# Kernel optimization log

Hardware: AMD Instinct MI355X
Metric: run time of the kernel (lower is better)

## Reference

```python
import jax, jax.numpy as jnp
import numpy as np

N_FEATURES = 200
KERNEL = 50
N_WIN = N_FEATURES - KERNEL + 1  # 151 sub-vectors
HID_F = [100, 50]
HID_G = [50, 25]   # 0.5 * hidden_dims
REP = 128
BATCH = 2048
TAU = 0.01
BN_EPS = 1e-5


def _window_indices():
    start = np.arange(N_FEATURES)[:-KERNEL + 1]
    all_idx = start[:, None] + np.arange(KERNEL)                      # [N_WIN, KERNEL]
    comp = np.array([np.setdiff1d(np.arange(N_FEATURES), row) for row in all_idx])  # [N_WIN, N_FEATURES-KERNEL]
    return jnp.asarray(all_idx), jnp.asarray(comp)

ALL_IDX, COMP_IDX = _window_indices()


def setup_inputs() -> dict:
    key = jax.random.key(0)
    ks = jax.random.split(key, 8)
    def w(k, o, i):
        return jax.random.normal(k, (o, i), jnp.float32) / np.float32(np.sqrt(i))
    gd = [KERNEL] + HID_G + [REP]
    fd = [N_FEATURES - KERNEL] + HID_F + [REP]
    inp = {"x": jax.random.normal(ks[0], (BATCH, N_FEATURES), jnp.float32)}
    inp["gW0"] = w(ks[1], gd[1], gd[0])
    inp["gW1"] = w(ks[2], gd[2], gd[1])
    inp["gW2"] = w(ks[3], gd[3], gd[2])
    inp["fW0"] = w(ks[4], fd[1], fd[0])
    inp["fW1"] = w(ks[5], fd[2], fd[1])
    inp["fW2"] = w(ks[6], fd[3], fd[2])
    # torch.randperm(n_pos)[:min(max_negatives, n_pos)] with max_negatives=1000 > 151
    inp["negative_index"] = jax.random.permutation(ks[7], jnp.arange(N_WIN))
    return inp


def _bn(h):
    # BatchNorm1d on [B, C, F]: training-mode stats over (batch, feature), affine=False (bias=False)
    m = h.mean(axis=(0, 2), keepdims=True)
    v = ((h - m) ** 2).mean(axis=(0, 2), keepdims=True)
    return (h - m) * jax.lax.rsqrt(v + BN_EPS)


def _leaky(h):
    return jnp.where(h >= 0, h, 0.01 * h)


def _mlp(h, Ws, acts):
    # LinearBlock: linear (no bias) -> batchnorm -> activation, every layer incl. last
    for W, a in zip(Ws, acts):
        h = a(_bn(h @ W.T))
    return h


def _normalize_dim1(h):
    # F.normalize default dim=1 (over the window dim of [B, N_WIN, REP]), eps=1e-12
    n = jnp.sqrt((h * h).sum(axis=1, keepdims=True))
    return h / jnp.maximum(n, 1e-12)


def reference(x, gW0, gW1, gW2, fW0, fW1, fW2, negative_index):
    # positive_matrix_builder: pure gathers instead of repeat + fancy indexing
    x1 = x[:, ALL_IDX]    # [B, N_WIN, KERNEL]
    x2 = x[:, COMP_IDX]   # [B, N_WIN, N_FEATURES-KERNEL]
    pos = _normalize_dim1(_mlp(x1, [gW0, gW1, gW2], [_leaky, _leaky, _leaky]))        # enc_g
    query = _normalize_dim1(_mlp(x2, [fW0, fW1, fW2], [jnp.tanh, _leaky, _leaky]))    # enc_f
    # cal_logit
    pos_mult = (query * pos).sum(axis=-1, keepdims=True)                 # [B, N_WIN, 1]
    neg = jnp.einsum('bnd,bmd->bnm', query, pos)[:, :, negative_index]  # [B, N_WIN, N_WIN]
    mask = (jnp.eye(N_WIN, dtype=jnp.float32)[:, negative_index] == 1)[None]
    neg = jnp.where(mask, -jnp.inf, neg)
    logit = jnp.concatenate([pos_mult, neg], axis=-1) / TAU              # [B, N_WIN, 1+N_WIN]
    return jnp.transpose(logit, (0, 2, 1))                               # [B, 1+N_WIN, N_WIN]
```

## Files before the change

### kernel.cpp

```cpp
#include <hip/hip_runtime.h>
#include <math.h>
#include <string.h>

constexpr int BB   = 2048;
constexpr int NW   = 151;
constexpr int NF   = 200;
constexpr float BN_EPS = 1e-5f;


typedef __bf16 bf16x8 __attribute__((ext_vector_type(8)));
typedef float  f32x4  __attribute__((ext_vector_type(4)));
typedef unsigned short u16x8 __attribute__((ext_vector_type(8)));

__device__ __forceinline__ unsigned short f2bf(float f) {
  unsigned int u; memcpy(&u, &f, 4);
  unsigned int r = (u + 0x7FFFu + ((u >> 16) & 1u)) >> 16;
  return (unsigned short)r;
}
__device__ __forceinline__ float bf2f(unsigned short u) {
  unsigned int x = ((unsigned int)u) << 16;
  float f; memcpy(&f, &x, 4);
  return f;
}

__global__ __launch_bounds__(256) void f1scan_k(
  const float* __restrict__ x, const float* __restrict__ W,
  float* __restrict__ Df)
{
  __shared__ float Wt[150*51];
  __shared__ float xs[800];
  __shared__ float lso[3200];
  const int t  = threadIdx.x;
  const int b0 = blockIdx.x * 4;
  const int ch = blockIdx.y;
  const int bl = t >> 6;
  const int c  = t & 63;

  for (int idx = t; idx < 50*150; idx += 256) {
    int cl = idx / 150, k = idx % 150;
    Wt[k*51 + cl] = W[(ch*50 + cl)*150 + k];
  }
  for (int idx = t; idx < 800; idx += 256) {
    int b2 = idx / 200, j = idx % 200;
    xs[idx] = x[(b0 + b2)*200 + j];
  }
  __syncthreads();

  float h = 0.f;
  if (c < 50) {
    #pragma unroll 5
    for (int i = 0; i < 150; i++)
      h += Wt[i*51 + c] * xs[bl*200 + 50 + i];
  }

  for (int n0 = 0; n0 < NW; n0 += 16) {
    const int cs = (NW - n0 < 16) ? (NW - n0) : 16;
    if (c < 50) {
      for (int l = 0; l < cs; l++) {
        int n = n0 + l;
        lso[bl*800 + l*50 + c] = h;
        if (n < 150) h += Wt[n*51 + c] * (xs[bl*200 + n] - xs[bl*200 + n + 50]);
      }
    }
    __syncthreads();
    const int tot = 4*cs*50;
    for (int idx = t; idx < tot; idx += 256) {
      int b2 = idx / (cs*50), rem = idx % (cs*50);
      int l = rem / 50, cc = rem % 50;
      Df[((size_t)(n0 + l)*BB + (b0 + b2))*100 + ch*50 + cc] = lso[b2*800 + l*50 + cc];
    }
    __syncthreads();
  }
}

template<int C>
__global__ __launch_bounds__(256) void bnstats_k(
  const float* __restrict__ H, float* __restrict__ stats)
{
  __shared__ float red[8];
  const int n = blockIdx.x, b0 = blockIdx.y * 256, t = threadIdx.x;
  const float* base = H + (size_t)n*BB*C + (size_t)b0*C;
  float s1 = 0.f, s2 = 0.f;
  for (int idx = t; idx < 256*C; idx += 256) {
    float v = base[idx];
    s1 += v; s2 += v*v;
  }
  #pragma unroll
  for (int off = 32; off; off >>= 1) {
    s1 += __shfl_down(s1, off); s2 += __shfl_down(s2, off);
  }
  if ((t & 63) == 0) { red[(t>>6)*2] = s1; red[(t>>6)*2+1] = s2; }
  __syncthreads();
  if (t == 0) {
    atomicAdd(&stats[2*n],   red[0]+red[2]+red[4]+red[6]);
    atomicAdd(&stats[2*n+1], red[1]+red[3]+red[5]+red[7]);
  }
}

__global__ __launch_bounds__(256) void wcvt_k(
  const float* __restrict__ W, unsigned short* __restrict__ Wb,
  int OUT, int IN, int KP, int total)
{
  int idx = blockIdx.x*256 + threadIdx.x;
  if (idx >= total) return;
  int o = idx / KP, k = idx % KP;
  float v = (o < OUT && k < IN) ? W[o*IN + k] : 0.f;
  unsigned short hi = f2bf(v);
  float lo = v - bf2f(hi);
  Wb[idx] = hi;
  Wb[total + idx] = f2bf(lo);
}

template<int IN, int OUT, int MODE, int ACT>
__global__ __launch_bounds__(256) void layer_mfma_k(
    const float* __restrict__ X, const unsigned short* __restrict__ Wb,
    const float* __restrict__ statsPrev, float* __restrict__ H,
    float* __restrict__ statsOut)
{
  constexpr int KP   = (IN + 31) & ~31;
  constexpr int OUTP = (OUT + 15) & ~15;
  constexpr int KC   = KP / 32;
  constexpr int NT   = OUTP / 16;
  constexpr int MT   = 2;

  __shared__ float red[8];
  const int n    = blockIdx.x;
  const int b0   = blockIdx.y * 128;
  const int t    = threadIdx.x;
  const int w    = t >> 6;
  const int lane = t & 63;
  const int l16  = lane & 15;
  const int quad = lane >> 4;

  float mean = 0.f, rstd = 1.f;
  if constexpr (MODE == 2) {
    const float cnt = (float)BB * (float)IN;
    mean = statsPrev[2*n] / cnt;
    float var = statsPrev[2*n+1] / cnt - mean*mean;
    rstd = rsqrtf(var + BN_EPS);
  }

  bf16x8 af_hi[MT][KC], af_lo[MT][KC];
  #pragma unroll
  for (int mt = 0; mt < MT; mt++) {
    const int bb = b0 + (w*MT + mt)*16 + l16;
    const float* xr = (MODE == 0)
        ? (X + (size_t)bb*NF + n)
        : (X + ((size_t)n*BB + bb)*IN);
    #pragma unroll
    for (int kc = 0; kc < KC; kc++) {
      const int k0 = kc*32 + quad*8;
      float vv[8];
      if constexpr (MODE == 0) {
        #pragma unroll
        for (int j = 0; j < 8; j++) {
          int k = k0 + j;
          vv[j] = (k < IN) ? xr[k] : 0.f;
        }
      } else if constexpr (IN % 4 == 0) {
        #pragma unroll
        for (int g = 0; g < 2; g++) {
          int kg = k0 + 4*g;
          if (kg < IN) {
            float4 f = *(const float4*)(xr + kg);
            vv[4*g] = f.x; vv[4*g+1] = f.y; vv[4*g+2] = f.z; vv[4*g+3] = f.w;
          } else {
            vv[4*g] = 0.f; vv[4*g+1] = 0.f; vv[4*g+2] = 0.f; vv[4*g+3] = 0.f;
          }
        }
      } else if constexpr (IN % 2 == 0) {
        #pragma unroll
        for (int g = 0; g < 4; g++) {
          int kg = k0 + 2*g;
          if (kg < IN) {
            float2 f = *(const float2*)(xr + kg);
            vv[2*g] = f.x; vv[2*g+1] = f.y;
          } else {
            vv[2*g] = 0.f; vv[2*g+1] = 0.f;
          }
        }
      } else {
        #pragma unroll
        for (int j = 0; j < 8; j++) {
          int k = k0 + j;
          vv[j] = (k < IN) ? xr[k] : 0.f;
        }
      }
      u16x8 hi, lo;
      #pragma unroll
      for (int j = 0; j < 8; j++) {
        bool valid = (k0 + j) < IN;
        float v;
        if constexpr (MODE == 0) {
          v = vv[j];
        } else {
          float z = (vv[j] - mean) * rstd;
          float a = (ACT == 1) ? ((z >= 0.f) ? z : 0.01f*z) : tanhf(z);
          v = valid ? a : 0.f;
        }
        unsigned short h16 = f2bf(v);
        hi[j] = h16;
        lo[j] = f2bf(v - bf2f(h16));
      }
      af_hi[mt][kc] = __builtin_bit_cast(bf16x8, hi);
      af_lo[mt][kc] = __builtin_bit_cast(bf16x8, lo);
    }
  }

  float s1 = 0.f, s2 = 0.f;
  #pragma unroll
  for (int nt = 0; nt < NT; nt++) {
    const int c = nt*16 + l16;
    f32x4 acc[MT];
    #pragma unroll
    for (int mt = 0; mt < MT; mt++) acc[mt] = (f32x4){0.f, 0.f, 0.f, 0.f};
    #pragma unroll
    for (int kc = 0; kc < KC; kc++) {
      const unsigned short* wp = Wb + (size_t)(nt*16 + l16)*KP + kc*32 + quad*8;
      bf16x8 wh = *(const bf16x8*)wp;
      bf16x8 wl = *(const bf16x8*)(wp + OUTP*KP);
      #pragma unroll
      for (int mt = 0; mt < MT; mt++) {
        acc[mt] = __builtin_amdgcn_mfma_f32_16x16x32_bf16(af_hi[mt][kc], wh, acc[mt], 0, 0, 0);
        acc[mt] = __builtin_amdgcn_mfma_f32_16x16x32_bf16(af_lo[mt][kc], wh, acc[mt], 0, 0, 0);
        acc[mt] = __builtin_amdgcn_mfma_f32_16x16x32_bf16(af_hi[mt][kc], wl, acc[mt], 0, 0, 0);
      }
    }
    #pragma unroll
    for (int mt = 0; mt < MT; mt++) {
      const int mrow = (w*MT + mt)*16 + quad*4;
      #pragma unroll
      for (int r = 0; r < 4; r++) {
        float v = acc[mt][r];
        s1 += v; s2 += v*v;
        if (c < OUT)
          H[((size_t)n*BB + (b0 + mrow + r))*OUT + c] = v;
      }
    }
  }

  #pragma unroll
  for (int off = 32; off; off >>= 1) {
    s1 += __shfl_down(s1, off); s2 += __shfl_down(s2, off);
  }
  if (lane == 0) { red[w*2] = s1; red[w*2+1] = s2; }
  __syncthreads();
  if (t == 0) {
    atomicAdd(&statsOut[2*n],   red[0]+red[2]+red[4]+red[6]);
    atomicAdd(&statsOut[2*n+1], red[1]+red[3]+red[5]+red[7]);
  }
}

__global__ void mr_k(const float* __restrict__ sP, const float* __restrict__ sQ,
                     float* __restrict__ mrP, float* __restrict__ mrQ)
{
  int n = threadIdx.x;
  if (n >= NW) return;
  const float cnt = (float)BB * 128.f;
  float m = sP[2*n] / cnt;
  float var = sP[2*n+1] / cnt - m*m;
  mrP[2*n] = m; mrP[2*n+1] = rsqrtf(var + BN_EPS);
  m = sQ[2*n] / cnt;
  var = sQ[2*n+1] / cnt - m*m;
  mrQ[2*n] = m; mrQ[2*n+1] = rsqrtf(var + BN_EPS);
}

__global__ __launch_bounds__(256) void normstats_k(
  const float* __restrict__ H, const float* __restrict__ mr,
  float* __restrict__ rinv)
{
  int idx = blockIdx.x*256 + threadIdx.x;
  int b = idx >> 7, d = idx & 127;
  float s = 0.f;
  #pragma unroll 4
  for (int n = 0; n < NW; n++) {
    float m = mr[2*n];
    float r = mr[2*n+1];
    float v = H[((size_t)n*BB + b)*128 + d];
    float z = (v - m) * r;
    float lv = (z >= 0.f) ? z : 0.01f*z;
    s += lv*lv;
  }
  rinv[idx] = 1.f / fmaxf(sqrtf(s), 1e-12f);
}

__global__ void invperm_k(const int* __restrict__ perm, int* __restrict__ inv) {
  int j = threadIdx.x;
  if (j < NW) inv[perm[j]] = j;
}

__global__ __launch_bounds__(256) void fusedfinal_k(
  const float* __restrict__ P32, const float* __restrict__ Q32,
  const float* __restrict__ mrP, const float* __restrict__ mrQ,
  const float* __restrict__ rinvP, const float* __restrict__ rinvQ,
  const int* __restrict__ inv, float* __restrict__ out)
{
  __shared__ unsigned short Qf[40*64*8];
  __shared__ float stgbuf[4][16*154];
  __shared__ int invs[NW];

  const int b    = blockIdx.x;
  const int t    = threadIdx.x;
  const int w    = t >> 6;
  const int lane = t & 63;
  const int l16  = lane & 15;
  const int quad = lane >> 4;

  for (int i = t; i < NW; i += 256) invs[i] = inv[i];

  {
    const int kcw = w;
    const int c0  = kcw*32 + quad*8;
    float ri[8];
    {
      float4 r0 = *(const float4*)&rinvQ[(b<<7) + c0];
      float4 r1 = *(const float4*)&rinvQ[(b<<7) + c0 + 4];
      ri[0]=r0.x; ri[1]=r0.y; ri[2]=r0.z; ri[3]=r0.w;
      ri[4]=r1.x; ri[5]=r1.y; ri[6]=r1.z; ri[7]=r1.w;
    }
    #pragma unroll
    for (int tj = 0; tj < 10; tj++) {
      const int n = tj*16 + l16;
      u16x8 hh;
      if (n < NW) {
        const float mQ = mrQ[2*n];
        const float rQ = mrQ[2*n+1];
        const float* qrow = Q32 + ((size_t)n*BB + b)*128 + c0;
        float4 u0 = *(const float4*)qrow;
        float4 u1 = *(const float4*)(qrow + 4);
        float e[8] = {u0.x, u0.y, u0.z, u0.w, u1.x, u1.y, u1.z, u1.w};
        #pragma unroll
        for (int j = 0; j < 8; j++) {
          float z = (e[j] - mQ) * rQ;
          z = ((z >= 0.f) ? z : 0.01f*z) * ri[j];
          hh[j] = f2bf(z);
        }
      } else {
        #pragma unroll
        for (int j = 0; j < 8; j++) hh[j] = 0;
      }
      *(bf16x8*)(Qf + ((size_t)(tj*4 + kcw)*64 + lane)*8) =
          __builtin_bit_cast(bf16x8, hh);
    }
  }
  __syncthreads();

  float riA[4][8];
  #pragma unroll
  for (int kc = 0; kc < 4; kc++) {
    const int c0 = kc*32 + quad*8;
    float4 r0 = *(const float4*)&rinvP[(b<<7) + c0];
    float4 r1 = *(const float4*)&rinvP[(b<<7) + c0 + 4];
    riA[kc][0]=r0.x; riA[kc][1]=r0.y; riA[kc][2]=r0.z; riA[kc][3]=r0.w;
    riA[kc][4]=r1.x; riA[kc][5]=r1.y; riA[kc][6]=r1.z; riA[kc][7]=r1.w;
  }

  float* ob = out + (size_t)b*152*NW;
  float* stg = stgbuf[w];
  const float NEG_BIG = -3.0e38f;

  for (int ti = w; ti < 10; ti += 4) {
    const int mbase = ti*16;
    const int arow = (mbase + l16 < NW) ? (mbase + l16) : (NW-1);
    const float mP = mrP[2*arow];
    const float rP = mrP[2*arow+1];
    const float* prow = P32 + ((size_t)arow*BB + b)*128;
    bf16x8 af[4];
    #pragma unroll
    for (int kc = 0; kc < 4; kc++) {
      const int c0 = kc*32 + quad*8;
      float4 v0 = *(const float4*)(prow + c0);
      float4 v1 = *(const float4*)(prow + c0 + 4);
      float e[8] = {v0.x, v0.y, v0.z, v0.w, v1.x, v1.y, v1.z, v1.w};
      u16x8 hh;
      #pragma unroll
      for (int j = 0; j < 8; j++) {
        float z = (e[j] - mP) * rP;
        z = ((z >= 0.f) ? z : 0.01f*z) * riA[kc][j];
        hh[j] = f2bf(z);
      }
      af[kc] = __builtin_bit_cast(bf16x8, hh);
    }

    #pragma unroll 2
    for (int tj = 0; tj < 10; tj++) {
      f32x4 acc = {0.f, 0.f, 0.f, 0.f};
      #pragma unroll
      for (int kc = 0; kc < 4; kc++) {
        bf16x8 bf = *(const bf16x8*)(Qf + ((size_t)(tj*4 + kc)*64 + lane)*8);
        acc = __builtin_amdgcn_mfma_f32_16x16x32_bf16(af[kc], bf, acc, 0, 0, 0);
      }
      const int col = tj*16 + l16;
      if (col < NW) {
        #pragma unroll
        for (int r = 0; r < 4; r++)
          stg[(quad*4 + r)*154 + col] = acc[r];
      }
    }
    for (int r = 0; r < 16; r++) {
      const int mm = mbase + r;
      if (mm >= NW) break;
      const int orow = 1 + invs[mm];
      float* dst = ob + (size_t)orow*NW;
      for (int col = lane; col < NW; col += 64) {
        float v = stg[r*154 + col] * 100.f;
        if (col == mm) { ob[mm] = v; v = NEG_BIG; }
        dst[col] = v;
      }
    }
  }
}

extern "C" void kernel_launch(void* const* d_in, const int* in_sizes, int n_in,
                              void* d_out, int out_size, void* d_ws, size_t ws_size,
                              hipStream_t stream) {
  const float* x   = (const float*)d_in[0];
  const float* gW0 = (const float*)d_in[1];
  const float* gW1 = (const float*)d_in[2];
  const float* gW2 = (const float*)d_in[3];
  const float* fW0 = (const float*)d_in[4];
  const float* fW1 = (const float*)d_in[5];
  const float* fW2 = (const float*)d_in[6];
  const int*  perm = (const int*)d_in[7];
  float* out = (float*)d_out;
  char* ws = (char*)d_ws;

  float* stats = (float*)ws;
  int*   inv   = (int*)(ws + 8192);
  float* mrP   = (float*)(ws + 10240);
  float* mrQ   = (float*)(ws + 11648);
  float* rinvP = (float*)(ws + 16384);
  float* rinvQ = rinvP + 2048*128;
  float* Ag = (float*)(ws + 16384 + 2*1048576);
  float* Bg = Ag + 15462400;
  float* Cg = Bg + 7731200;
  float* Df = Cg + 39583744;
  float* Ff = Df + 30924800;
  float* Ef = Ag;

  unsigned short* Wbase = (unsigned short*)(ws + 16384);
  unsigned short* Wg1 = Wbase;
  unsigned short* Wg2 = Wbase + 8192;
  unsigned short* Wg3 = Wbase + 12288;
  unsigned short* Wf2 = Wbase + 20480;
  unsigned short* Wf3 = Wbase + 36864;

  float* sg1 = stats,        *sg2 = stats + 302,  *sg3 = stats + 604;
  float* sf1 = stats + 906,  *sf2 = stats + 1208, *sf3 = stats + 1510;

  hipMemsetAsync(stats, 0, 1812*sizeof(float), stream);
  invperm_k<<<1, 192, 0, stream>>>(perm, inv);

  wcvt_k<<<16, 256, 0, stream>>>(gW0, Wg1,  50,  50,  64, 4096);
  wcvt_k<<< 8, 256, 0, stream>>>(gW1, Wg2,  25,  50,  64, 2048);
  wcvt_k<<<16, 256, 0, stream>>>(gW2, Wg3, 128,  25,  32, 4096);
  wcvt_k<<<32, 256, 0, stream>>>(fW1, Wf2,  50, 100, 128, 8192);
  wcvt_k<<<32, 256, 0, stream>>>(fW2, Wf3, 128,  50,  64, 8192);

  f1scan_k<<<dim3(BB/4, 2), 256, 0, stream>>>(x, fW0, Df);
  bnstats_k<100><<<dim3(NW, 8), 256, 0, stream>>>(Df, sf1);

  dim3 gl2(NW, BB/128);
  layer_mfma_k< 50,  50, 0, 0><<<gl2, 256, 0, stream>>>(x,  Wg1, nullptr, Ag, sg1);
  layer_mfma_k< 50,  25, 2, 1><<<gl2, 256, 0, stream>>>(Ag, Wg2, sg1,     Bg, sg2);
  layer_mfma_k< 25, 128, 2, 1><<<gl2, 256, 0, stream>>>(Bg, Wg3, sg2,     Cg, sg3);
  layer_mfma_k<100,  50, 2, 2><<<gl2, 256, 0, stream>>>(Df, Wf2, sf1,     Ef, sf2);
  layer_mfma_k< 50, 128, 2, 1><<<gl2, 256, 0, stream>>>(Ef, Wf3, sf2,     Ff, sf3);

  mr_k<<<1, 192, 0, stream>>>(sg3, sf3, mrP, mrQ);

  normstats_k<<<1024, 256, 0, stream>>>(Cg, mrP, rinvP);
  normstats_k<<<1024, 256, 0, stream>>>(Ff, mrQ, rinvQ);

  fusedfinal_k<<<BB, 256, 0, stream>>>(Cg, Ff, mrP, mrQ, rinvP, rinvQ, inv, out);
  (void)in_sizes; (void)n_in; (void)out_size; (void)ws_size;
}
```

Baseline: 806.4 us.

## Store final-layer activations as bf16, fuse BN stats into scan, merge weight conversion

The two 128-wide final-layer activation buffers are now written as bf16 instead of fp32, which halves the traffic for normstats and the final logit kernel that reads them. The separate bnstats pass over the first f-layer output is removed: f1scan now accumulates sum and sum of squares in shared memory with atomics and flushes them to global stats. The five weight-conversion launches are merged into one kernel, and the final kernel prefetches its first P row early. Storing pre-BN activations in bf16 adds rounding error ahead of normalisation, and the shared-memory atomics are heavily contended.

Result: slower. 1.050 ms (+30.2%).

```diff
diff --git a/kernel.cpp b/kernel.cpp
--- a/kernel.cpp
+++ b/kernel.cpp
@@ -25,17 +25,19 @@
 
 __global__ __launch_bounds__(256) void f1scan_k(
   const float* __restrict__ x, const float* __restrict__ W,
-  float* __restrict__ Df)
+  float* __restrict__ Df, float* __restrict__ stats)
 {
   __shared__ float Wt[150*51];
   __shared__ float xs[800];
   __shared__ float lso[3200];
+  __shared__ float redNS[32];
   const int t  = threadIdx.x;
   const int b0 = blockIdx.x * 4;
   const int ch = blockIdx.y;
   const int bl = t >> 6;
   const int c  = t & 63;
 
+  if (t < 32) redNS[t] = 0.f;
   for (int idx = t; idx < 50*150; idx += 256) {
     int cl = idx / 150, k = idx % 150;
     Wt[k*51 + cl] = W[(ch*50 + cl)*150 + k];
@@ -67,51 +69,46 @@
     for (int idx = t; idx < tot; idx += 256) {
       int b2 = idx / (cs*50), rem = idx % (cs*50);
       int l = rem / 50, cc = rem % 50;
-      Df[((size_t)(n0 + l)*BB + (b0 + b2))*100 + ch*50 + cc] = lso[b2*800 + l*50 + cc];
+      float v = lso[b2*800 + l*50 + cc];
+      Df[((size_t)(n0 + l)*BB + (b0 + b2))*100 + ch*50 + cc] = v;
+      atomicAdd(&redNS[l*2],   v);
+      atomicAdd(&redNS[l*2+1], v*v);
     }
     __syncthreads();
-  }
-}
-
-template<int C>
-__global__ __launch_bounds__(256) void bnstats_k(
-  const float* __restrict__ H, float* __restrict__ stats)
-{
-  __shared__ float red[8];
-  const int n = blockIdx.x, b0 = blockIdx.y * 256, t = threadIdx.x;
-  const float* base = H + (size_t)n*BB*C + (size_t)b0*C;
-  float s1 = 0.f, s2 = 0.f;
-  for (int idx = t; idx < 256*C; idx += 256) {
-    float v = base[idx];
-    s1 += v; s2 += v*v;
-  }
-  #pragma unroll
-  for (int off = 32; off; off >>= 1) {
-    s1 += __shfl_down(s1, off); s2 += __shfl_down(s2, off);
-  }
-  if ((t & 63) == 0) { red[(t>>6)*2] = s1; red[(t>>6)*2+1] = s2; }
-  __syncthreads();
-  if (t == 0) {
-    atomicAdd(&stats[2*n],   red[0]+red[2]+red[4]+red[6]);
-    atomicAdd(&stats[2*n+1], red[1]+red[3]+red[5]+red[7]);
-  }
-}
-
-__global__ __launch_bounds__(256) void wcvt_k(
+    if (t < 32) {
+      if (t < cs*2) atomicAdd(&stats[2*(n0 + (t >> 1)) + (t & 1)], redNS[t]);
+      redNS[t] = 0.f;
+    }
+    __syncthreads();
+  }
+}
+
+__device__ __forceinline__ void wcvt_one(
   const float* __restrict__ W, unsigned short* __restrict__ Wb,
-  int OUT, int IN, int KP, int total)
-{
-  int idx = blockIdx.x*256 + threadIdx.x;
+  int OUT, int IN, int KP, int total, int idx)
+{
   if (idx >= total) return;
   int o = idx / KP, k = idx % KP;
   float v = (o < OUT && k < IN) ? W[o*IN + k] : 0.f;
   unsigned short hi = f2bf(v);
-  float lo = v - bf2f(hi);
   Wb[idx] = hi;
-  Wb[total + idx] = f2bf(lo);
-}
-
-template<int IN, int OUT, int MODE, int ACT>
+  Wb[total + idx] = f2bf(v - bf2f(hi));
+}
+
+__global__ __launch_bounds__(256) void wcvt_all_k(
+  const float* __restrict__ gW0, const float* __restrict__ gW1,
+  const float* __restrict__ gW2, const float* __restrict__ fW1,
+  const float* __restrict__ fW2, unsigned short* __restrict__ Wbase)
+{
+  int bid = blockIdx.x, t = threadIdx.x;
+  if (bid < 16)       wcvt_one(gW0, Wbase,          50,  50,  64, 4096, (bid      )*256 + t);
+  else if (bid < 24)  wcvt_one(gW1, Wbase + 8192,   25,  50,  64, 2048, (bid - 16 )*256 + t);
+  else if (bid < 40)  wcvt_one(gW2, Wbase + 12288, 128,  25,  32, 4096, (bid - 24 )*256 + t);
+  else if (bid < 72)  wcvt_one(fW1, Wbase + 20480,  50, 100, 128, 8192, (bid - 40 )*256 + t);
+  else                wcvt_one(fW2, Wbase + 36864, 128,  50,  64, 8192, (bid - 72 )*256 + t);
+}
+
+template<int IN, int OUT, int MODE, int ACT, bool OUTBF>
 __global__ __launch_bounds__(256) void layer_mfma_k(
     const float* __restrict__ X, const unsigned short* __restrict__ Wb,
     const float* __restrict__ statsPrev, float* __restrict__ H,
@@ -233,8 +230,11 @@
       for (int r = 0; r < 4; r++) {
         float v = acc[mt][r];
         s1 += v; s2 += v*v;
-        if (c < OUT)
-          H[((size_t)n*BB + (b0 + mrow + r))*OUT + c] = v;
+        if (c < OUT) {
+          size_t off = ((size_t)n*BB + (b0 + mrow + r))*OUT + c;
+          if constexpr (OUTBF) ((unsigned short*)H)[off] = f2bf(v);
+          else                 H[off] = v;
+        }
       }
     }
   }
@@ -266,7 +266,7 @@
 }
 
 __global__ __launch_bounds__(256) void normstats_k(
-  const float* __restrict__ H, const float* __restrict__ mr,
+  const unsigned short* __restrict__ H, const float* __restrict__ mr,
   float* __restrict__ rinv)
 {
   int idx = blockIdx.x*256 + threadIdx.x;
@@ -276,7 +276,7 @@
   for (int n = 0; n < NW; n++) {
     float m = mr[2*n];
     float r = mr[2*n+1];
-    float v = H[((size_t)n*BB + b)*128 + d];
+    float v = bf2f(H[((size_t)n*BB + b)*128 + d]);
     float z = (v - m) * r;
     float lv = (z >= 0.f) ? z : 0.01f*z;
     s += lv*lv;
@@ -290,7 +290,7 @@
 }
 
 __global__ __launch_bounds__(256) void fusedfinal_k(
-  const float* __restrict__ P32, const float* __restrict__ Q32,
+  const unsigned short* __restrict__ Pb, const unsigned short* __restrict__ Qb,
   const float* __restrict__ mrP, const float* __restrict__ mrQ,
   const float* __restrict__ rinvP, const float* __restrict__ rinvQ,
   const int* __restrict__ inv, float* __restrict__ out)
@@ -307,6 +307,13 @@
   const int quad = lane >> 4;
 
   for (int i = t; i < NW; i += 256) invs[i] = inv[i];
+
+  const int arow0 = (w*16 + l16 < NW) ? (w*16 + l16) : (NW-1);
+  const unsigned short* prow0 = Pb + ((size_t)arow0*BB + b)*128;
+  u16x8 praw[4];
+  #pragma unroll
+  for (int kc = 0; kc < 4; kc++)
+    praw[kc] = *(const u16x8*)(prow0 + kc*32 + quad*8);
 
   {
     const int kcw = w;
@@ -325,13 +332,10 @@
       if (n < NW) {
         const float mQ = mrQ[2*n];
         const float rQ = mrQ[2*n+1];
-        const float* qrow = Q32 + ((size_t)n*BB + b)*128 + c0;
-        float4 u0 = *(const float4*)qrow;
-        float4 u1 = *(const float4*)(qrow + 4);
-        float e[8] = {u0.x, u0.y, u0.z, u0.w, u1.x, u1.y, u1.z, u1.w};
+        u16x8 uv = *(const u16x8*)(Qb + ((size_t)n*BB + b)*128 + c0);
         #pragma unroll
         for (int j = 0; j < 8; j++) {
-          float z = (e[j] - mQ) * rQ;
+          float z = (bf2f(uv[j]) - mQ) * rQ;
           z = ((z >= 0.f) ? z : 0.01f*z) * ri[j];
           hh[j] = f2bf(z);
         }
@@ -364,18 +368,16 @@
     const int arow = (mbase + l16 < NW) ? (mbase + l16) : (NW-1);
     const float mP = mrP[2*arow];
     const float rP = mrP[2*arow+1];
-    const float* prow = P32 + ((size_t)arow*BB + b)*128;
+    const unsigned short* prow = Pb + ((size_t)arow*BB + b)*128;
     bf16x8 af[4];
     #pragma unroll
     for (int kc = 0; kc < 4; kc++) {
-      const int c0 = kc*32 + quad*8;
-      float4 v0 = *(const float4*)(prow + c0);
-      float4 v1 = *(const float4*)(prow + c0 + 4);
-      float e[8] = {v0.x, v0.y, v0.z, v0.w, v1.x, v1.y, v1.z, v1.w};
+      u16x8 uv = (ti == w) ? praw[kc]
+                           : *(const u16x8*)(prow + kc*32 + quad*8);
       u16x8 hh;
       #pragma unroll
       for (int j = 0; j < 8; j++) {
-        float z = (e[j] - mP) * rP;
+        float z = (bf2f(uv[j]) - mP) * rP;
         z = ((z >= 0.f) ? z : 0.01f*z) * riA[kc][j];
         hh[j] = f2bf(z);
       }
@@ -437,13 +439,10 @@
   float* Df = Cg + 39583744;
   float* Ff = Df + 30924800;
   float* Ef = Ag;
+  unsigned short* Cgb = (unsigned short*)Cg;
+  unsigned short* Ffb = (unsigned short*)Ff;
 
   unsigned short* Wbase = (unsigned short*)(ws + 16384);
-  unsigned short* Wg1 = Wbase;
-  unsigned short* Wg2 = Wbase + 8192;
-  unsigned short* Wg3 = Wbase + 12288;
-  unsigned short* Wf2 = Wbase + 20480;
-  unsigned short* Wf3 = Wbase + 36864;
 
   float* sg1 = stats,        *sg2 = stats + 302,  *sg3 = stats + 604;
   float* sf1 = stats + 906,  *sf2 = stats + 1208, *sf3 = stats + 1510;
@@ -451,27 +450,22 @@
   hipMemsetAsync(stats, 0, 1812*sizeof(float), stream);
   invperm_k<<<1, 192, 0, stream>>>(perm, inv);
 
-  wcvt_k<<<16, 256, 0, stream>>>(gW0, Wg1,  50,  50,  64, 4096);
-  wcvt_k<<< 8, 256, 0, stream>>>(gW1, Wg2,  25,  50,  64, 2048);
-  wcvt_k<<<16, 256, 0, stream>>>(gW2, Wg3, 128,  25,  32, 4096);
-  wcvt_k<<<32, 256, 0, stream>>>(fW1, Wf2,  50, 100, 128, 8192);
-  wcvt_k<<<32, 256, 0, stream>>>(fW2, Wf3, 128,  50,  64, 8192);
-
-  f1scan_k<<<dim3(BB/4, 2), 256, 0, stream>>>(x, fW0, Df);
-  bnstats_k<100><<<dim3(NW, 8), 256, 0, stream>>>(Df, sf1);
+  wcvt_all_k<<<104, 256, 0, stream>>>(gW0, gW1, gW2, fW1, fW2, Wbase);
+
+  f1scan_k<<<dim3(BB/4, 2), 256, 0, stream>>>(x, fW0, Df, sf1);
 
   dim3 gl2(NW, BB/128);
-  layer_mfma_k< 50,  50, 0, 0><<<gl2, 256, 0, stream>>>(x,  Wg1, nullptr, Ag, sg1);
-  layer_mfma_k< 50,  25, 2, 1><<<gl2, 256, 0, stream>>>(Ag, Wg2, sg1,     Bg, sg2);
-  layer_mfma_k< 25, 128, 2, 1><<<gl2, 256, 0, stream>>>(Bg, Wg3, sg2,     Cg, sg3);
-  layer_mfma_k<100,  50, 2, 2><<<gl2, 256, 0, stream>>>(Df, Wf2, sf1,     Ef, sf2);
-  layer_mfma_k< 50, 128, 2, 1><<<gl2, 256, 0, stream>>>(Ef, Wf3, sf2,     Ff, sf3);
+  layer_mfma_k< 50,  50, 0, 0, false><<<gl2, 256, 0, stream>>>(x,  Wbase,         nullptr, Ag, sg1);
+  layer_mfma_k< 50,  25, 2, 1, false><<<gl2, 256, 0, stream>>>(Ag, Wbase + 8192,  sg1,     Bg, sg2);
+  layer_mfma_k< 25, 128, 2, 1, true ><<<gl2, 256, 0, stream>>>(Bg, Wbase + 12288, sg2,     Cg, sg3);
+  layer_mfma_k<100,  50, 2, 2, false><<<gl2, 256, 0, stream>>>(Df, Wbase + 20480, sf1,     Ef, sf2);
+  layer_mfma_k< 50, 128, 2, 1, true ><<<gl2, 256, 0, stream>>>(Ef, Wbase + 36864, sf2,     Ff, sf3);
 
   mr_k<<<1, 192, 0, stream>>>(sg3, sf3, mrP, mrQ);
 
-  normstats_k<<<1024, 256, 0, stream>>>(Cg, mrP, rinvP);
-  normstats_k<<<1024, 256, 0, stream>>>(Ff, mrQ, rinvQ);
-
-  fusedfinal_k<<<BB, 256, 0, stream>>>(Cg, Ff, mrP, mrQ, rinvP, rinvQ, inv, out);
+  normstats_k<<<1024, 256, 0, stream>>>(Cgb, mrP, rinvP);
+  normstats_k<<<1024, 256, 0, stream>>>(Ffb, mrQ, rinvQ);
+
+  fusedfinal_k<<<BB, 256, 0, stream>>>(Cgb, Ffb, mrP, mrQ, rinvP, rinvQ, inv, out);
   (void)in_sizes; (void)n_in; (void)out_size; (void)ws_size;
 }
```
